# Optimization experiments

Hardware: AMD Instinct MI355X
Metric: run time of the kernel (lower is better)

The kernel has to match this reference:

```python
import jax, jax.numpy as jnp
import numpy as np

B, T, I = 8192, 20, 16
H1, H2, FC = 128, 64, 32


def _lstm(x_tbi, Wih, Whh, bih, bhh, H):
    """PyTorch-convention LSTM. x_tbi: (T,B,in). Gate order: i,f,g,o. Returns (T,B,H) hidden seq."""
    Tn, Bn = x_tbi.shape[0], x_tbi.shape[1]
    # precompute input projection for all timesteps: (T,B,4H)
    xz = jnp.einsum('tbi,gi->tbg', x_tbi, Wih) + (bih + bhh)

    def step(carry, xz_t):
        h, c = carry
        z = xz_t + h @ Whh.T  # (B,4H)
        i = jax.nn.sigmoid(z[:, 0*H:1*H])
        f = jax.nn.sigmoid(z[:, 1*H:2*H])
        g = jnp.tanh(z[:, 2*H:3*H])
        o = jax.nn.sigmoid(z[:, 3*H:4*H])
        c = f * c + i * g
        h = o * jnp.tanh(c)
        return (h, c), h

    h0 = jnp.zeros((Bn, H), x_tbi.dtype)
    c0 = jnp.zeros((Bn, H), x_tbi.dtype)
    _, hs = jax.lax.scan(step, (h0, c0), xz)
    return hs  # (T,B,H)


def setup_inputs() -> dict:
    key = jax.random.key(0)
    ks = jax.random.split(key, 16)
    s1 = 1.0 / np.sqrt(H1)
    s2 = 1.0 / np.sqrt(H2)
    u = lambda k, shape, s: jax.random.uniform(k, shape, jnp.float32, -s, s)
    return {
        'x': jax.random.normal(ks[0], (B, T, I), jnp.float32),
        'Wih1': u(ks[1], (4 * H1, I), s1),
        'Whh1': u(ks[2], (4 * H1, H1), s1),
        'bih1': u(ks[3], (4 * H1,), s1),
        'bhh1': u(ks[4], (4 * H1,), s1),
        'Wih2': u(ks[5], (4 * H2, H1), s2),
        'Whh2': u(ks[6], (4 * H2, H2), s2),
        'bih2': u(ks[7], (4 * H2,), s2),
        'bhh2': u(ks[8], (4 * H2,), s2),
        'gamma': jnp.ones((H2,), jnp.float32),
        'beta': jnp.zeros((H2,), jnp.float32),
        'W1': u(ks[9], (FC, H2), 1.0 / np.sqrt(H2)),
        'b1': u(ks[10], (FC,), 1.0 / np.sqrt(H2)),
        'W2': u(ks[11], (1, FC), 1.0 / np.sqrt(FC)),
        'b2': u(ks[12], (1,), 1.0 / np.sqrt(FC)),
    }


def reference(x, Wih1, Whh1, bih1, bhh1, Wih2, Whh2, bih2, bhh2, gamma, beta, W1, b1, W2, b2):
    # dropout layers are identity (eval mode)
    x_tbi = jnp.transpose(x, (1, 0, 2))           # (T,B,I)
    out1 = _lstm(x_tbi, Wih1, Whh1, bih1, bhh1, H1)  # (T,B,H1)
    out2 = _lstm(out1, Wih2, Whh2, bih2, bhh2, H2)   # (T,B,H2)
    last = out2[-1]                               # (B,H2)
    # LayerNorm over H2
    mu = jnp.mean(last, axis=-1, keepdims=True)
    var = jnp.mean((last - mu) ** 2, axis=-1, keepdims=True)
    normed = (last - mu) * jax.lax.rsqrt(var + 1e-5) * gamma + beta
    h = jax.nn.relu(normed @ W1.T + b1)           # (B,FC)
    logit = h @ W2.T + b2                         # (B,1)
    return logit[:, 0]
```

## Files before the change

### kernel.cpp

```cpp
#include <hip/hip_runtime.h>

#define TS 20
#define BATCH 8192

typedef _Float16 half8 __attribute__((ext_vector_type(8)));
typedef float f32x4 __attribute__((ext_vector_type(4)));

__device__ __forceinline__ float fast_sig(float z) {
    return __builtin_amdgcn_rcpf(1.0f + __expf(-z));
}
__device__ __forceinline__ float fast_tanh(float z) {
    return 1.0f - 2.0f * __builtin_amdgcn_rcpf(1.0f + __expf(2.0f * z));
}

extern "C" __global__ __launch_bounds__(512, 2)
void lstm1_kernel(const float* __restrict__ x,
                  const float* __restrict__ Wih1, const float* __restrict__ Whh1,
                  const float* __restrict__ bih1, const float* __restrict__ bhh1,
                  _Float16* __restrict__ out1)
{
    __shared__ __align__(16) _Float16 Hb[2][2][16][128];
    __shared__ __align__(16) _Float16 Xb[32][672];

    const int tid  = threadIdx.x;
    const int lane = tid & 63;
    const int w    = tid >> 6;
    const int lrow = lane & 15;
    const int lgrp = lane >> 4;
    const int b0   = blockIdx.x * 32;

    half8 bf[4][5];
    float bias[4];
#pragma unroll
    for (int g = 0; g < 4; ++g) {
        const int n = g * 128 + w * 16 + lrow;
        bias[g] = bih1[n] + bhh1[n];
#pragma unroll
        for (int ch = 0; ch < 5; ++ch) {
            half8 v;
#pragma unroll
            for (int j = 0; j < 8; ++j) {
                const int kk = ch * 32 + lgrp * 8 + j;
                float t;
                if (kk < 128)      t = Whh1[n * 128 + kk];
                else if (kk < 144) t = Wih1[n * 16 + (kk - 128)];
                else               t = 0.0f;
                v[j] = (_Float16)t;
            }
            bf[g][ch] = v;
        }
    }

    for (int i = tid; i < 32 * 672; i += 512) (&Xb[0][0])[i] = (_Float16)0.0f;
    for (int i = tid; i < 2 * 2 * 16 * 128; i += 512) (&Hb[0][0][0][0])[i] = (_Float16)0.0f;
    __syncthreads();
    for (int i = tid; i < 32 * 320; i += 512) {
        const int r = i / 320, k = i % 320;
        const int t = k >> 4, ii = k & 15;
        const int u = (t * 4 + (ii >> 3)) ^ (r & 7);
        Xb[r][u * 8 + (ii & 7)] = (_Float16)x[(size_t)(b0 + r) * 320 + k];
    }
    __syncthreads();

    float c1[2][4] = {{0.f,0.f,0.f,0.f},{0.f,0.f,0.f,0.f}};

    const int srow = tid >> 4;
    const int sc   = tid & 15;
    const int stile = srow >> 4, srr = srow & 15;
    const size_t out_off = (size_t)(b0 + srow) * 128 + sc * 8;

    for (int tt = 0; tt < 10; ++tt) {
#pragma unroll
        for (int p = 0; p < 2; ++p) {
            const int t = tt * 2 + p;
            half8 a[2][5];
#pragma unroll
            for (int tile = 0; tile < 2; ++tile) {
#pragma unroll
                for (int ch = 0; ch < 4; ++ch)
                    a[tile][ch] = *(const half8*)&Hb[p ^ 1][tile][lrow][(((ch << 2) | lgrp) ^ (lrow & 7)) * 8];
                const int r = tile * 16 + lrow;
                a[tile][4] = *(const half8*)&Xb[r][((t * 4 + lgrp) ^ (lrow & 7)) * 8];
            }
            f32x4 z[2][4];
#pragma unroll
            for (int tile = 0; tile < 2; ++tile)
#pragma unroll
                for (int g = 0; g < 4; ++g) {
                    f32x4 acc = {bias[g], bias[g], bias[g], bias[g]};
#pragma unroll
                    for (int ch = 0; ch < 5; ++ch)
                        acc = __builtin_amdgcn_mfma_f32_16x16x32_f16(a[tile][ch], bf[g][ch], acc, 0, 0, 0);
                    z[tile][g] = acc;
                }
#pragma unroll
            for (int tile = 0; tile < 2; ++tile)
#pragma unroll
                for (int j = 0; j < 4; ++j) {
                    const float iv = fast_sig (z[tile][0][j]);
                    const float fv = fast_sig (z[tile][1][j]);
                    const float gv = fast_tanh(z[tile][2][j]);
                    const float ov = fast_sig (z[tile][3][j]);
                    const float cn = fv * c1[tile][j] + iv * gv;
                    c1[tile][j] = cn;
                    const float h = ov * fast_tanh(cn);
                    const int m  = (lgrp << 2) | j;
                    const int cu = ((w * 2 + (lrow >> 3)) ^ (m & 7));
                    Hb[p][tile][m][cu * 8 + (lrow & 7)] = (_Float16)h;
                }
            __syncthreads();
            {
                const half8 v = *(const half8*)&Hb[p][stile][srr][((sc ^ (srr & 7)) * 8)];
                *(half8*)(out1 + (size_t)t * (BATCH * 128) + out_off) = v;
            }
        }
    }
}

extern "C" __global__ __launch_bounds__(256, 2)
void lstm2_head_kernel(const _Float16* __restrict__ out1,
                       const float* __restrict__ Wih2, const float* __restrict__ Whh2,
                       const float* __restrict__ bih2, const float* __restrict__ bhh2,
                       const float* __restrict__ gamma, const float* __restrict__ beta,
                       const float* __restrict__ W1fc, const float* __restrict__ b1fc,
                       const float* __restrict__ W2fc, const float* __restrict__ b2fc,
                       float* __restrict__ out)
{
    __shared__ __align__(16) _Float16 A2h1[2][16][128];
    __shared__ __align__(16) _Float16 A2h2[2][16][72];
    __shared__ float h2f[16][68];
    __shared__ float nrm[16][68];

    const int tid  = threadIdx.x;
    const int lane = tid & 63;
    const int w    = tid >> 6;
    const int lrow = lane & 15;
    const int lgrp = lane >> 4;
    const int b0   = blockIdx.x * 16;

    half8 bf2[4][6];
    float bias2[4];
#pragma unroll
    for (int g = 0; g < 4; ++g) {
        const int n = g * 64 + w * 16 + lrow;
        bias2[g] = bih2[n] + bhh2[n];
#pragma unroll
        for (int ch = 0; ch < 6; ++ch) {
            half8 v;
#pragma unroll
            for (int j = 0; j < 8; ++j) {
                const int kk = ch * 32 + lgrp * 8 + j;
                v[j] = (_Float16)((kk < 128) ? Wih2[n * 128 + kk]
                                             : Whh2[n * 64 + (kk - 128)]);
            }
            bf2[g][ch] = v;
        }
    }

    for (int i = tid; i < 16 * 72 * 2; i += 256)
        (&A2h2[0][0][0])[i] = (_Float16)0.0f;

    const int prow = tid >> 4, pck = tid & 15;
    {
        const half8 v = *(const half8*)(out1 + ((size_t)(b0 + prow)) * 128 + pck * 8);
        *(half8*)&A2h1[0][prow][((pck ^ (prow & 7)) * 8)] = v;
    }
    half8 pf1 = *(const half8*)(out1 + ((size_t)1 * BATCH + b0 + prow) * 128 + pck * 8);
    half8 pf2 = *(const half8*)(out1 + ((size_t)2 * BATCH + b0 + prow) * 128 + pck * 8);

    float c2[4] = {0.f, 0.f, 0.f, 0.f};
    __syncthreads();

    int cur = 0;
    for (int t = 0; t < TS; ++t) {
        const int nxt = cur ^ 1;
        f32x4 z[4];
#pragma unroll
        for (int g = 0; g < 4; ++g) {
            f32x4 acc = {bias2[g], bias2[g], bias2[g], bias2[g]};
#pragma unroll
            for (int ch = 0; ch < 6; ++ch) {
                half8 a;
                if (ch < 4) {
                    const int ckr = (ch * 4 + lgrp) ^ (lrow & 7);
                    a = *(const half8*)&A2h1[cur][lrow][ckr * 8];
                } else {
                    a = *(const half8*)&A2h2[cur][lrow][(ch - 4) * 32 + lgrp * 8];
                }
                acc = __builtin_amdgcn_mfma_f32_16x16x32_f16(a, bf2[g][ch], acc, 0, 0, 0);
            }
            z[g] = acc;
        }
        const int cell = w * 16 + lrow;
#pragma unroll
        for (int j = 0; j < 4; ++j) {
            const float iv = fast_sig (z[0][j]);
            const float fv = fast_sig (z[1][j]);
            const float gv = fast_tanh(z[2][j]);
            const float ov = fast_sig (z[3][j]);
            const float cn = fv * c2[j] + iv * gv;
            c2[j] = cn;
            const float h = ov * fast_tanh(cn);
            const int m = lgrp * 4 + j;
            A2h2[nxt][m][cell] = (_Float16)h;
            if (t == TS - 1) h2f[m][cell] = h;
        }
        if (t + 1 < TS)
            *(half8*)&A2h1[nxt][prow][((pck ^ (prow & 7)) * 8)] = pf1;
        pf1 = pf2;
        if (t + 3 < TS)
            pf2 = *(const half8*)(out1 + ((size_t)(t + 3) * BATCH + b0 + prow) * 128 + pck * 8);
        __syncthreads();
        cur = nxt;
    }

    {
        const int m = tid >> 4, q = tid & 15;
        const float v0 = h2f[m][q * 4 + 0];
        const float v1 = h2f[m][q * 4 + 1];
        const float v2 = h2f[m][q * 4 + 2];
        const float v3 = h2f[m][q * 4 + 3];
        float s = v0 + v1 + v2 + v3;
        s += __shfl_xor(s, 1); s += __shfl_xor(s, 2);
        s += __shfl_xor(s, 4); s += __shfl_xor(s, 8);
        const float mean = s * (1.0f / 64.0f);
        const float d0 = v0 - mean, d1 = v1 - mean, d2 = v2 - mean, d3 = v3 - mean;
        float vs = d0 * d0 + d1 * d1 + d2 * d2 + d3 * d3;
        vs += __shfl_xor(vs, 1); vs += __shfl_xor(vs, 2);
        vs += __shfl_xor(vs, 4); vs += __shfl_xor(vs, 8);
        const float rstd = rsqrtf(vs * (1.0f / 64.0f) + 1e-5f);
        const int i0 = q * 4;
        nrm[m][i0 + 0] = d0 * rstd * gamma[i0 + 0] + beta[i0 + 0];
        nrm[m][i0 + 1] = d1 * rstd * gamma[i0 + 1] + beta[i0 + 1];
        nrm[m][i0 + 2] = d2 * rstd * gamma[i0 + 2] + beta[i0 + 2];
        nrm[m][i0 + 3] = d3 * rstd * gamma[i0 + 3] + beta[i0 + 3];
    }
    __syncthreads();
    {
        const int o = tid & 31;
        const int mbase = tid >> 5;
#pragma unroll
        for (int rr = 0; rr < 2; ++rr) {
            const int m = mbase + rr * 8;
            float acc = b1fc[o];
#pragma unroll 8
            for (int k = 0; k < 64; ++k) acc += nrm[m][k] * W1fc[o * 64 + k];
            const float hv = fmaxf(acc, 0.0f);
            float p = hv * W2fc[o];
            p += __shfl_xor(p, 1); p += __shfl_xor(p, 2);
            p += __shfl_xor(p, 4); p += __shfl_xor(p, 8); p += __shfl_xor(p, 16);
            if (o == 0) out[b0 + m] = p + b2fc[0];
        }
    }
}

extern "C" void kernel_launch(void* const* d_in, const int* in_sizes, int n_in,
                              void* d_out, int out_size, void* d_ws, size_t ws_size,
                              hipStream_t stream) {
    (void)in_sizes; (void)n_in; (void)ws_size; (void)out_size;
    const float* x_p    = (const float*)d_in[0];
    const float* Wih1_p = (const float*)d_in[1];
    const float* Whh1_p = (const float*)d_in[2];
    const float* bih1_p = (const float*)d_in[3];
    const float* bhh1_p = (const float*)d_in[4];
    const float* Wih2_p = (const float*)d_in[5];
    const float* Whh2_p = (const float*)d_in[6];
    const float* bih2_p = (const float*)d_in[7];
    const float* bhh2_p = (const float*)d_in[8];
    const float* gamma_p = (const float*)d_in[9];
    const float* beta_p  = (const float*)d_in[10];
    const float* W1_p   = (const float*)d_in[11];
    const float* b1_p   = (const float*)d_in[12];
    const float* W2_p   = (const float*)d_in[13];
    const float* b2_p   = (const float*)d_in[14];
    float* out_p = (float*)d_out;

    _Float16* out1 = (_Float16*)d_ws;

    lstm1_kernel<<<dim3(BATCH / 32), dim3(512), 0, stream>>>(
        x_p, Wih1_p, Whh1_p, bih1_p, bhh1_p, out1);
    lstm2_head_kernel<<<dim3(BATCH / 16), dim3(256), 0, stream>>>(
        out1, Wih2_p, Whh2_p, bih2_p, bhh2_p,
        gamma_p, beta_p, W1_p, b1_p, W2_p, b2_p, out_p);
}
```

Before: 95.23 us.

## Halve LSTM1 batch tile, fold log2e into weights, reorder MFMA loops

LSTM1 now processes 16 batch rows per block instead of 32, which doubles the grid and raises the launch bound to 4 blocks per CU so more recurrent chains run concurrently. Gate weights and biases are pre-scaled by log2(e) (twice that for the tanh gate), so the activations can use raw exp2 without a multiply. The MFMA loops are restructured so each A fragment is loaded once and reused across the four gates, and the LDS swizzle and LSTM2 padding are adjusted. Each block now carries less work for the same fixed per-step sync and weight-load overhead, and the fp16 weights are scaled before conversion, which slightly changes rounding.

```diff
diff --git a/kernel.cpp b/kernel.cpp
--- a/kernel.cpp
+++ b/kernel.cpp
@@ -2,115 +2,121 @@
 
 #define TS 20
 #define BATCH 8192
+#define LOG2E 1.4426950408889634f
 
 typedef _Float16 half8 __attribute__((ext_vector_type(8)));
 typedef float f32x4 __attribute__((ext_vector_type(4)));
 
-__device__ __forceinline__ float fast_sig(float z) {
-    return __builtin_amdgcn_rcpf(1.0f + __expf(-z));
-}
-__device__ __forceinline__ float fast_tanh(float z) {
-    return 1.0f - 2.0f * __builtin_amdgcn_rcpf(1.0f + __expf(2.0f * z));
-}
-
-extern "C" __global__ __launch_bounds__(512, 2)
+__device__ __forceinline__ float fexp2(float x) {
+#if __has_builtin(__builtin_amdgcn_exp2f)
+    return __builtin_amdgcn_exp2f(x);
+#else
+    return exp2f(x);
+#endif
+}
+__device__ __forceinline__ float sig2(float zp) {
+    return __builtin_amdgcn_rcpf(1.0f + fexp2(-zp));
+}
+__device__ __forceinline__ float tanh2(float zp) {
+    return 1.0f - 2.0f * __builtin_amdgcn_rcpf(1.0f + fexp2(zp));
+}
+__device__ __forceinline__ int swz(int r) { return (r & 7) ^ (((r >> 3) & 1) << 2); }
+
+extern "C" __global__ __launch_bounds__(512, 4)
 void lstm1_kernel(const float* __restrict__ x,
                   const float* __restrict__ Wih1, const float* __restrict__ Whh1,
                   const float* __restrict__ bih1, const float* __restrict__ bhh1,
                   _Float16* __restrict__ out1)
 {
-    __shared__ __align__(16) _Float16 Hb[2][2][16][128];
-    __shared__ __align__(16) _Float16 Xb[32][672];
+    __shared__ __align__(16) _Float16 Hb[2][16][128];
+    __shared__ __align__(16) _Float16 Xb[16][640];
 
     const int tid  = threadIdx.x;
     const int lane = tid & 63;
     const int w    = tid >> 6;
     const int lrow = lane & 15;
     const int lgrp = lane >> 4;
-    const int b0   = blockIdx.x * 32;
+    const int b0   = blockIdx.x * 16;
 
     half8 bf[4][5];
     float bias[4];
 #pragma unroll
     for (int g = 0; g < 4; ++g) {
+        const float sc = (g == 2) ? 2.0f * LOG2E : LOG2E;
         const int n = g * 128 + w * 16 + lrow;
-        bias[g] = bih1[n] + bhh1[n];
+        bias[g] = (bih1[n] + bhh1[n]) * sc;
 #pragma unroll
         for (int ch = 0; ch < 5; ++ch) {
             half8 v;
-#pragma unroll
-            for (int j = 0; j < 8; ++j) {
-                const int kk = ch * 32 + lgrp * 8 + j;
-                float t;
-                if (kk < 128)      t = Whh1[n * 128 + kk];
-                else if (kk < 144) t = Wih1[n * 16 + (kk - 128)];
-                else               t = 0.0f;
-                v[j] = (_Float16)t;
+            if (ch < 4) {
+                const float4 p0 = *(const float4*)&Whh1[n * 128 + ch * 32 + lgrp * 8];
+                const float4 p1 = *(const float4*)&Whh1[n * 128 + ch * 32 + lgrp * 8 + 4];
+                v[0]=(_Float16)(p0.x*sc); v[1]=(_Float16)(p0.y*sc); v[2]=(_Float16)(p0.z*sc); v[3]=(_Float16)(p0.w*sc);
+                v[4]=(_Float16)(p1.x*sc); v[5]=(_Float16)(p1.y*sc); v[6]=(_Float16)(p1.z*sc); v[7]=(_Float16)(p1.w*sc);
+            } else if (lgrp < 2) {
+                const float4 p0 = *(const float4*)&Wih1[n * 16 + lgrp * 8];
+                const float4 p1 = *(const float4*)&Wih1[n * 16 + lgrp * 8 + 4];
+                v[0]=(_Float16)(p0.x*sc); v[1]=(_Float16)(p0.y*sc); v[2]=(_Float16)(p0.z*sc); v[3]=(_Float16)(p0.w*sc);
+                v[4]=(_Float16)(p1.x*sc); v[5]=(_Float16)(p1.y*sc); v[6]=(_Float16)(p1.z*sc); v[7]=(_Float16)(p1.w*sc);
+            } else {
+#pragma unroll
+                for (int j = 0; j < 8; ++j) v[j] = (_Float16)0.0f;
             }
             bf[g][ch] = v;
         }
     }
 
-    for (int i = tid; i < 32 * 672; i += 512) (&Xb[0][0])[i] = (_Float16)0.0f;
-    for (int i = tid; i < 2 * 2 * 16 * 128; i += 512) (&Hb[0][0][0][0])[i] = (_Float16)0.0f;
-    __syncthreads();
-    for (int i = tid; i < 32 * 320; i += 512) {
+    for (int i = tid; i < 16 * 640; i += 512) (&Xb[0][0])[i] = (_Float16)0.0f;
+    for (int i = tid; i < 2 * 16 * 128; i += 512) (&Hb[0][0][0])[i] = (_Float16)0.0f;
+    __syncthreads();
+    for (int i = tid; i < 16 * 320; i += 512) {
         const int r = i / 320, k = i % 320;
         const int t = k >> 4, ii = k & 15;
-        const int u = (t * 4 + (ii >> 3)) ^ (r & 7);
+        const int u = (t * 4 + (ii >> 3)) ^ swz(r);
         Xb[r][u * 8 + (ii & 7)] = (_Float16)x[(size_t)(b0 + r) * 320 + k];
     }
     __syncthreads();
 
-    float c1[2][4] = {{0.f,0.f,0.f,0.f},{0.f,0.f,0.f,0.f}};
-
-    const int srow = tid >> 4;
-    const int sc   = tid & 15;
-    const int stile = srow >> 4, srr = srow & 15;
-    const size_t out_off = (size_t)(b0 + srow) * 128 + sc * 8;
+    float c1[4] = {0.f, 0.f, 0.f, 0.f};
+    const int hu   = w * 2 + (lrow >> 3);
+    const int hlo  = lrow & 7;
+    const int sz   = swz(lrow);
+
+    const int srow = (tid >> 4) & 15;
+    const int sc_  = tid & 15;
+    const size_t out_off = (size_t)(b0 + srow) * 128 + sc_ * 8;
 
     for (int tt = 0; tt < 10; ++tt) {
 #pragma unroll
         for (int p = 0; p < 2; ++p) {
             const int t = tt * 2 + p;
-            half8 a[2][5];
-#pragma unroll
-            for (int tile = 0; tile < 2; ++tile) {
-#pragma unroll
-                for (int ch = 0; ch < 4; ++ch)
-                    a[tile][ch] = *(const half8*)&Hb[p ^ 1][tile][lrow][(((ch << 2) | lgrp) ^ (lrow & 7)) * 8];
-                const int r = tile * 16 + lrow;
-                a[tile][4] = *(const half8*)&Xb[r][((t * 4 + lgrp) ^ (lrow & 7)) * 8];
-            }
-            f32x4 z[2][4];
-#pragma unroll
-            for (int tile = 0; tile < 2; ++tile)
-#pragma unroll
-                for (int g = 0; g < 4; ++g) {
-                    f32x4 acc = {bias[g], bias[g], bias[g], bias[g]};
-#pragma unroll
-                    for (int ch = 0; ch < 5; ++ch)
-                        acc = __builtin_amdgcn_mfma_f32_16x16x32_f16(a[tile][ch], bf[g][ch], acc, 0, 0, 0);
-                    z[tile][g] = acc;
-                }
-#pragma unroll
-            for (int tile = 0; tile < 2; ++tile)
-#pragma unroll
-                for (int j = 0; j < 4; ++j) {
-                    const float iv = fast_sig (z[tile][0][j]);
-                    const float fv = fast_sig (z[tile][1][j]);
-                    const float gv = fast_tanh(z[tile][2][j]);
-                    const float ov = fast_sig (z[tile][3][j]);
-                    const float cn = fv * c1[tile][j] + iv * gv;
-                    c1[tile][j] = cn;
-                    const float h = ov * fast_tanh(cn);
-                    const int m  = (lgrp << 2) | j;
-                    const int cu = ((w * 2 + (lrow >> 3)) ^ (m & 7));
-                    Hb[p][tile][m][cu * 8 + (lrow & 7)] = (_Float16)h;
-                }
+            f32x4 z[4];
+#pragma unroll
+            for (int g = 0; g < 4; ++g) z[g] = (f32x4){bias[g], bias[g], bias[g], bias[g]};
+#pragma unroll
+            for (int ch = 0; ch < 5; ++ch) {
+                half8 a;
+                if (ch < 4) a = *(const half8*)&Hb[p ^ 1][lrow][(((ch << 2) | lgrp) ^ sz) * 8];
+                else        a = *(const half8*)&Xb[lrow][((((t << 2) | lgrp)) ^ sz) * 8];
+#pragma unroll
+                for (int g = 0; g < 4; ++g)
+                    z[g] = __builtin_amdgcn_mfma_f32_16x16x32_f16(a, bf[g][ch], z[g], 0, 0, 0);
+            }
+#pragma unroll
+            for (int j = 0; j < 4; ++j) {
+                const float iv = sig2 (z[0][j]);
+                const float fv = sig2 (z[1][j]);
+                const float gv = tanh2(z[2][j]);
+                const float ov = sig2 (z[3][j]);
+                const float cn = fv * c1[j] + iv * gv;
+                c1[j] = cn;
+                const float h = ov * tanh2(2.0f * LOG2E * cn);
+                const int m = (lgrp << 2) | j;
+                Hb[p][m][((hu ^ swz(m)) << 3) | hlo] = (_Float16)h;
+            }
             __syncthreads();
-            {
-                const half8 v = *(const half8*)&Hb[p][stile][srr][((sc ^ (srr & 7)) * 8)];
+            if (tid < 256) {
+                const half8 v = *(const half8*)&Hb[p][srow][((sc_ ^ swz(srow)) << 3)];
                 *(half8*)(out1 + (size_t)t * (BATCH * 128) + out_off) = v;
             }
         }
@@ -127,7 +133,7 @@
                        float* __restrict__ out)
 {
     __shared__ __align__(16) _Float16 A2h1[2][16][128];
-    __shared__ __align__(16) _Float16 A2h2[2][16][72];
+    __shared__ __align__(16) _Float16 A2h2[2][16][76];
     __shared__ float h2f[16][68];
     __shared__ float nrm[16][68];
 
@@ -142,22 +148,23 @@
     float bias2[4];
 #pragma unroll
     for (int g = 0; g < 4; ++g) {
+        const float sc = (g == 2) ? 2.0f * LOG2E : LOG2E;
         const int n = g * 64 + w * 16 + lrow;
-        bias2[g] = bih2[n] + bhh2[n];
+        bias2[g] = (bih2[n] + bhh2[n]) * sc;
 #pragma unroll
         for (int ch = 0; ch < 6; ++ch) {
             half8 v;
-#pragma unroll
-            for (int j = 0; j < 8; ++j) {
-                const int kk = ch * 32 + lgrp * 8 + j;
-                v[j] = (_Float16)((kk < 128) ? Wih2[n * 128 + kk]
-                                             : Whh2[n * 64 + (kk - 128)]);
-            }
+            const float4 p0 = (ch < 4) ? *(const float4*)&Wih2[n * 128 + ch * 32 + lgrp * 8]
+                                       : *(const float4*)&Whh2[n * 64 + (ch - 4) * 32 + lgrp * 8];
+            const float4 p1 = (ch < 4) ? *(const float4*)&Wih2[n * 128 + ch * 32 + lgrp * 8 + 4]
+                                       : *(const float4*)&Whh2[n * 64 + (ch - 4) * 32 + lgrp * 8 + 4];
+            v[0]=(_Float16)(p0.x*sc); v[1]=(_Float16)(p0.y*sc); v[2]=(_Float16)(p0.z*sc); v[3]=(_Float16)(p0.w*sc);
+            v[4]=(_Float16)(p1.x*sc); v[5]=(_Float16)(p1.y*sc); v[6]=(_Float16)(p1.z*sc); v[7]=(_Float16)(p1.w*sc);
             bf2[g][ch] = v;
         }
     }
 
-    for (int i = tid; i < 16 * 72 * 2; i += 256)
+    for (int i = tid; i < 2 * 16 * 76; i += 256)
         (&A2h2[0][0][0])[i] = (_Float16)0.0f;
 
     const int prow = tid >> 4, pck = tid & 15;
@@ -176,32 +183,27 @@
         const int nxt = cur ^ 1;
         f32x4 z[4];
 #pragma unroll
-        for (int g = 0; g < 4; ++g) {
-            f32x4 acc = {bias2[g], bias2[g], bias2[g], bias2[g]};
-#pragma unroll
-            for (int ch = 0; ch < 6; ++ch) {
-                half8 a;
-                if (ch < 4) {
-                    const int ckr = (ch * 4 + lgrp) ^ (lrow & 7);
-                    a = *(const half8*)&A2h1[cur][lrow][ckr * 8];
-                } else {
-                    a = *(const half8*)&A2h2[cur][lrow][(ch - 4) * 32 + lgrp * 8];
-                }
-                acc = __builtin_amdgcn_mfma_f32_16x16x32_f16(a, bf2[g][ch], acc, 0, 0, 0);
-            }
-            z[g] = acc;
+        for (int g = 0; g < 4; ++g) z[g] = (f32x4){bias2[g], bias2[g], bias2[g], bias2[g]};
+#pragma unroll
+        for (int ch = 0; ch < 6; ++ch) {
+            half8 a;
+            if (ch < 4) a = *(const half8*)&A2h1[cur][lrow][(((ch << 2) | lgrp) ^ (lrow & 7)) * 8];
+            else        a = *(const half8*)&A2h2[cur][lrow][(ch - 4) * 32 + lgrp * 8];
+#pragma unroll
+            for (int g = 0; g < 4; ++g)
+                z[g] = __builtin_amdgcn_mfma_f32_16x16x32_f16(a, bf2[g][ch], z[g], 0, 0, 0);
         }
         const int cell = w * 16 + lrow;
 #pragma unroll
         for (int j = 0; j < 4; ++j) {
-            const float iv = fast_sig (z[0][j]);
-            const float fv = fast_sig (z[1][j]);
-            const float gv = fast_tanh(z[2][j]);
-            const float ov = fast_sig (z[3][j]);
+            const float iv = sig2 (z[0][j]);
+            const float fv = sig2 (z[1][j]);
+            const float gv = tanh2(z[2][j]);
+            const float ov = sig2 (z[3][j]);
             const float cn = fv * c2[j] + iv * gv;
             c2[j] = cn;
-            const float h = ov * fast_tanh(cn);
-            const int m = lgrp * 4 + j;
+            const float h = ov * tanh2(2.0f * LOG2E * cn);
+            const int m = (lgrp << 2) | j;
             A2h2[nxt][m][cell] = (_Float16)h;
             if (t == TS - 1) h2f[m][cell] = h;
         }
@@ -277,7 +279,7 @@
 
     _Float16* out1 = (_Float16*)d_ws;
 
-    lstm1_kernel<<<dim3(BATCH / 32), dim3(512), 0, stream>>>(
+    lstm1_kernel<<<dim3(BATCH / 16), dim3(512), 0, stream>>>(
         x_p, Wih1_p, Whh1_p, bih1_p, bhh1_p, out1);
     lstm2_head_kernel<<<dim3(BATCH / 16), dim3(256), 0, stream>>>(
         out1, Wih2_p, Whh2_p, bih2_p, bhh2_p,
```

Result: slower. 114.3 us (+20.0%).
